# Kernel tuning notes

Measured on AMD Instinct MI355X. Metric: run time of the kernel, lower is better.

## Reference

```python
import jax, jax.numpy as jnp
import numpy as np

IN_F = 4096
OUT_F = 4096
BLOCK = 16      # weight values decoded per latent code
D_LAT = 16      # latent dim per code
HID = 64        # decoder hidden width
K = 65536       # codebook size
NB = IN_F * OUT_F // BLOCK  # 1,048,576 blocks


def setup_inputs() -> dict:
    key = jax.random.key(0)
    ks = jax.random.split(key, 10)
    return {
        "x": jax.random.normal(ks[0], (4, 2048, IN_F), jnp.float32),
        "y_in_idx": jax.random.randint(ks[1], (NB,), 0, K),
        "codebook": jax.random.normal(ks[2], (K, D_LAT), jnp.float32) * 0.1,
        "W1": jax.random.normal(ks[3], (D_LAT, HID), jnp.float32) * 0.1,
        "b1": jnp.zeros((HID,), jnp.float32),
        "W2": jax.random.normal(ks[4], (HID, BLOCK), jnp.float32) * 0.1,
        "b2": jnp.zeros((BLOCK,), jnp.float32),
        "scale": jax.random.uniform(ks[5], (OUT_F,), jnp.float32, 0.5, 1.5),
        "shift": jax.random.normal(ks[6], (OUT_F,), jnp.float32) * 0.01,
        "bias": jax.random.normal(ks[7], (OUT_F,), jnp.float32) * 0.02,
    }


def reference(x, y_in_idx, codebook, W1, b1, W2, b2, scale, shift, bias):
    # 1) gather latent codes for every weight block: [NB, D_LAT]
    codes = codebook[y_in_idx]
    # 2) decode latents -> weight blocks via small MLP (comp_W_from_y analogue)
    h = jax.nn.relu(codes @ W1 + b1)          # [NB, HID]
    blocks = h @ W2 + b2                      # [NB, BLOCK]
    # 3) assemble reconstructed (standardized) weight hatWr: [OUT_F, IN_F]
    Wr = blocks.reshape(OUT_F, IN_F)
    # 4) de-standardize with per-output-row metadata (de_standardize_Wr)
    W_hat = Wr * scale[:, None] + shift[:, None]
    # 5) F.linear(input, W_hat, bias): [B, S, OUT_F]
    return jnp.einsum('bsi,oi->bso', x, W_hat) + bias
```

## Files before the change

### kernel.cpp

```cpp
#include <hip/hip_runtime.h>
#include <hip/hip_bf16.h>

#define IN_F   4096
#define OUT_F  4096
#define HID    64
#define D_LAT  16
#define BLK    16
#define NB     (IN_F * OUT_F / BLK)
#define NCODES 65536
#define M_TOT  8192
#define K_TOT  IN_F
#define N_TOT  OUT_F

typedef __bf16 bf16x8 __attribute__((ext_vector_type(8)));
typedef float  f32x4  __attribute__((ext_vector_type(4)));

__global__ __launch_bounds__(256) void convert_x_kernel(
    const float* __restrict__ x, __hip_bfloat16* __restrict__ xb) {
  size_t i = ((size_t)blockIdx.x * 256 + threadIdx.x) * 8;
  const float4* p = (const float4*)(x + i);
  float4 a = p[0], b = p[1];
  union { __hip_bfloat16 h[8]; uint4 q; } u;
  u.h[0] = __float2bfloat16(a.x); u.h[1] = __float2bfloat16(a.y);
  u.h[2] = __float2bfloat16(a.z); u.h[3] = __float2bfloat16(a.w);
  u.h[4] = __float2bfloat16(b.x); u.h[5] = __float2bfloat16(b.y);
  u.h[6] = __float2bfloat16(b.z); u.h[7] = __float2bfloat16(b.w);
  *(uint4*)(xb + i) = u.q;
}

__global__ __launch_bounds__(256) void decode_table_kernel(
    const float* __restrict__ codebook,
    const float* __restrict__ W1, const float* __restrict__ b1,
    const float* __restrict__ W2, const float* __restrict__ b2,
    float* __restrict__ table) {
  __shared__ __align__(16) __hip_bfloat16 sH[4][16 * 72];
  const int lane = threadIdx.x & 63;
  const int wave = threadIdx.x >> 6;
  const int n = lane & 15;
  const int q = lane >> 4;
  const bool act = q < 2;

  union { __hip_bfloat16 h[8]; bf16x8 v; } uz;
#pragma unroll
  for (int j = 0; j < 8; j++) uz.h[j] = __float2bfloat16(0.f);
  const bf16x8 zf = uz.v;
  const f32x4 z4 = (f32x4){0.f, 0.f, 0.f, 0.f};

  bf16x8 frag1[4];
#pragma unroll
  for (int g = 0; g < 4; g++) {
    union { __hip_bfloat16 h[8]; bf16x8 v; } u;
#pragma unroll
    for (int j = 0; j < 8; j++) {
      int k = (q * 8 + j) & 15;
      float w = act ? W1[k * HID + g * 16 + n] : 0.f;
      u.h[j] = __float2bfloat16(w);
    }
    frag1[g] = u.v;
  }
  bf16x8 frag2[2];
#pragma unroll
  for (int kk = 0; kk < 2; kk++) {
    union { __hip_bfloat16 h[8]; bf16x8 v; } u;
#pragma unroll
    for (int j = 0; j < 8; j++)
      u.h[j] = __float2bfloat16(W2[(kk * 32 + q * 8 + j) * BLK + n]);
    frag2[kk] = u.v;
  }
  float b1v[4];
#pragma unroll
  for (int g = 0; g < 4; g++) b1v[g] = b1[g * 16 + n];
  const float b2v = b2[n];

  const int c0w = blockIdx.x * 256 + wave * 64;
#pragma unroll 1
  for (int i = 0; i < 4; i++) {
    const int cbase = c0w + i * 16;
    const int id = cbase + n;
    const float4* cp = (const float4*)(codebook + (size_t)id * D_LAT + (q & 1) * 8);
    float4 ca = cp[0], cb = cp[1];
    union { __hip_bfloat16 h[8]; bf16x8 v; } ua;
    ua.h[0] = __float2bfloat16(ca.x); ua.h[1] = __float2bfloat16(ca.y);
    ua.h[2] = __float2bfloat16(ca.z); ua.h[3] = __float2bfloat16(ca.w);
    ua.h[4] = __float2bfloat16(cb.x); ua.h[5] = __float2bfloat16(cb.y);
    ua.h[6] = __float2bfloat16(cb.z); ua.h[7] = __float2bfloat16(cb.w);
    bf16x8 afrag = act ? ua.v : zf;

    f32x4 hC[4];
#pragma unroll
    for (int g = 0; g < 4; g++)
      hC[g] = __builtin_amdgcn_mfma_f32_16x16x32_bf16(afrag, frag1[g], z4, 0, 0, 0);

    __syncthreads();
#pragma unroll
    for (int g = 0; g < 4; g++)
#pragma unroll
      for (int r = 0; r < 4; r++) {
        float hv = fmaxf(hC[g][r] + b1v[g], 0.f);
        sH[wave][(q * 4 + r) * 72 + g * 16 + n] = __float2bfloat16(hv);
      }
    __syncthreads();

    bf16x8 a2_0 = *(const bf16x8*)&sH[wave][n * 72 + q * 8];
    bf16x8 a2_1 = *(const bf16x8*)&sH[wave][n * 72 + 32 + q * 8];
    f32x4 o4 = __builtin_amdgcn_mfma_f32_16x16x32_bf16(a2_0, frag2[0], z4, 0, 0, 0);
    o4 = __builtin_amdgcn_mfma_f32_16x16x32_bf16(a2_1, frag2[1], o4, 0, 0, 0);

#pragma unroll
    for (int r = 0; r < 4; r++) {
      int code = cbase + q * 4 + r;
      table[(size_t)code * BLK + n] = o4[r] + b2v;
    }
  }
}

__global__ __launch_bounds__(256) void gather_scale_kernel(
    const int* __restrict__ yidx, const float* __restrict__ table,
    const float* __restrict__ scale, const float* __restrict__ shift,
    __hip_bfloat16* __restrict__ What) {
  const int b = blockIdx.x * 256 + threadIdx.x;
  const int o = blockIdx.x;
  const float sc = scale[o], sh = shift[o];
  const int id = yidx[b];
  const float4* t = (const float4*)(table + (size_t)id * BLK);
  float4 v0 = t[0], v1 = t[1], v2 = t[2], v3 = t[3];
  union { __hip_bfloat16 h[16]; uint4 q[2]; } u;
  u.h[0]  = __float2bfloat16(v0.x * sc + sh);
  u.h[1]  = __float2bfloat16(v0.y * sc + sh);
  u.h[2]  = __float2bfloat16(v0.z * sc + sh);
  u.h[3]  = __float2bfloat16(v0.w * sc + sh);
  u.h[4]  = __float2bfloat16(v1.x * sc + sh);
  u.h[5]  = __float2bfloat16(v1.y * sc + sh);
  u.h[6]  = __float2bfloat16(v1.z * sc + sh);
  u.h[7]  = __float2bfloat16(v1.w * sc + sh);
  u.h[8]  = __float2bfloat16(v2.x * sc + sh);
  u.h[9]  = __float2bfloat16(v2.y * sc + sh);
  u.h[10] = __float2bfloat16(v2.z * sc + sh);
  u.h[11] = __float2bfloat16(v2.w * sc + sh);
  u.h[12] = __float2bfloat16(v3.x * sc + sh);
  u.h[13] = __float2bfloat16(v3.y * sc + sh);
  u.h[14] = __float2bfloat16(v3.z * sc + sh);
  u.h[15] = __float2bfloat16(v3.w * sc + sh);
  uint4* dst = (uint4*)(What + (size_t)b * BLK);
  dst[0] = u.q[0];
  dst[1] = u.q[1];
}

__device__ inline void gload_lds16(const void* g, void* l) {
  __builtin_amdgcn_global_load_lds(
      (const __attribute__((address_space(1))) void*)g,
      (__attribute__((address_space(3))) void*)l, 16, 0, 0);
}

__global__ __launch_bounds__(256, 2) void gemm_bt_kernel(
    const __hip_bfloat16* __restrict__ A, const __hip_bfloat16* __restrict__ B,
    const float* __restrict__ bias, float* __restrict__ C) {
  __shared__ __align__(16) __hip_bfloat16 sA[256 * 32];
  __shared__ __align__(16) __hip_bfloat16 sB[128 * 32];
  const int lane = threadIdx.x & 63;
  const int wave = threadIdx.x >> 6;
  const int m0 = blockIdx.y * 256;
  const int n0 = blockIdx.x * 128;
  const int wr = wave >> 1;
  const int wc = wave & 1;

  const int srow = lane >> 2;
  const int schk = (lane & 3) ^ ((lane >> 3) & 3);
  const __hip_bfloat16* aSrc =
      A + (size_t)(m0 + wave * 64 + srow) * K_TOT + schk * 8;
  const __hip_bfloat16* bSrc =
      B + (size_t)(n0 + wave * 32 + srow) * K_TOT + schk * 8;

  const int fl = lane & 15;
  const int pos = (lane >> 4) ^ ((fl >> 1) & 3);
  const __hip_bfloat16* aRd = &sA[(wr * 128 + fl) * 32 + pos * 8];
  const __hip_bfloat16* bRd = &sB[(wc * 64 + fl) * 32 + pos * 8];

  f32x4 acc[8][4];
#pragma unroll
  for (int i = 0; i < 8; i++)
#pragma unroll
    for (int j = 0; j < 4; j++) acc[i][j] = (f32x4){0.f, 0.f, 0.f, 0.f};

  for (int k0 = 0; k0 < K_TOT; k0 += 32) {
#pragma unroll
    for (int i = 0; i < 4; i++)
      gload_lds16(aSrc + (size_t)i * 16 * K_TOT + k0,
                  (char*)sA + (wave * 4 + i) * 1024);
#pragma unroll
    for (int i = 0; i < 2; i++)
      gload_lds16(bSrc + (size_t)i * 16 * K_TOT + k0,
                  (char*)sB + (wave * 2 + i) * 1024);
    __syncthreads();

    bf16x8 bf[4];
#pragma unroll
    for (int nt = 0; nt < 4; nt++) bf[nt] = *(const bf16x8*)(bRd + nt * 16 * 32);
#pragma unroll
    for (int mt = 0; mt < 8; mt++) {
      bf16x8 af = *(const bf16x8*)(aRd + mt * 16 * 32);
#pragma unroll
      for (int nt = 0; nt < 4; nt++)
        acc[mt][nt] = __builtin_amdgcn_mfma_f32_16x16x32_bf16(
            af, bf[nt], acc[mt][nt], 0, 0, 0);
    }
    __syncthreads();
  }

  float bs[4];
#pragma unroll
  for (int nt = 0; nt < 4; nt++) bs[nt] = bias[n0 + wc * 64 + nt * 16 + fl];
#pragma unroll
  for (int mt = 0; mt < 8; mt++) {
    int r0 = m0 + wr * 128 + mt * 16 + (lane >> 4) * 4;
#pragma unroll
    for (int nt = 0; nt < 4; nt++) {
      int cn = n0 + wc * 64 + nt * 16 + fl;
#pragma unroll
      for (int r = 0; r < 4; r++)
        C[(size_t)(r0 + r) * N_TOT + cn] = acc[mt][nt][r] + bs[nt];
    }
  }
}

extern "C" void kernel_launch(void* const* d_in, const int* in_sizes, int n_in,
                              void* d_out, int out_size, void* d_ws, size_t ws_size,
                              hipStream_t stream) {
  const float* x        = (const float*)d_in[0];
  const int*   yidx     = (const int*)d_in[1];
  const float* codebook = (const float*)d_in[2];
  const float* W1       = (const float*)d_in[3];
  const float* b1       = (const float*)d_in[4];
  const float* W2       = (const float*)d_in[5];
  const float* b2       = (const float*)d_in[6];
  const float* scale    = (const float*)d_in[7];
  const float* shift    = (const float*)d_in[8];
  const float* bias     = (const float*)d_in[9];
  float* out = (float*)d_out;

  __hip_bfloat16* What = (__hip_bfloat16*)d_ws;
  float* table = (float*)((char*)d_ws + (size_t)32 * 1024 * 1024);
  __hip_bfloat16* xb   = (__hip_bfloat16*)((char*)d_ws + (size_t)32 * 1024 * 1024);

  decode_table_kernel<<<NCODES / 256, 256, 0, stream>>>(codebook, W1, b1, W2, b2,
                                                        table);
  gather_scale_kernel<<<NB / 256, 256, 0, stream>>>(yidx, table, scale, shift, What);
  convert_x_kernel<<<(M_TOT * (size_t)K_TOT) / (256 * 8), 256, 0, stream>>>(x, xb);
  gemm_bt_kernel<<<dim3(N_TOT / 128, M_TOT / 256), 256, 0, stream>>>(xb, What, bias, out);
}
```

Before: 530.1 us.

## Replace GEMM with 256x256-tile double-buffered 8-phase pipelined kernel

Rewrites the bf16 GEMM to use 512-thread workgroups, 256x256 output tiles and a 64-wide K step. The main loop is double-buffered in 128KB of LDS and split into eight phases that interleave global-to-LDS staging with LDS reads and MFMA blocks, using raw barriers, waitcnt and setprio. It also remaps block IDs for L2 locality and uses an XOR-swizzled LDS layout. The aim is to hide global load latency and raise MFMA utilisation compared with the single-buffered loop, which synchronised twice per 32-wide K step. The cost is much higher LDS use per workgroup and fragile hand-written wait counts.

```diff
diff --git a/kernel.cpp b/kernel.cpp
--- a/kernel.cpp
+++ b/kernel.cpp
@@ -11,9 +11,14 @@
 #define M_TOT  8192
 #define K_TOT  IN_F
 #define N_TOT  OUT_F
+#define NT     (K_TOT / 64)
 
 typedef __bf16 bf16x8 __attribute__((ext_vector_type(8)));
 typedef float  f32x4  __attribute__((ext_vector_type(4)));
+
+#define S_BARRIER()  asm volatile("s_barrier" ::: "memory")
+#define WAIT_LGKM0() asm volatile("s_waitcnt lgkmcnt(0)" ::: "memory")
+#define WAIT_VM(n)   asm volatile("s_waitcnt vmcnt(" #n ")" ::: "memory")
 
 __global__ __launch_bounds__(256) void convert_x_kernel(
     const float* __restrict__ x, __hip_bfloat16* __restrict__ xb) {
@@ -152,75 +157,153 @@
       (__attribute__((address_space(3))) void*)l, 16, 0, 0);
 }
 
-__global__ __launch_bounds__(256, 2) void gemm_bt_kernel(
+__global__ __launch_bounds__(512, 2) void gemm_8ph_kernel(
     const __hip_bfloat16* __restrict__ A, const __hip_bfloat16* __restrict__ B,
     const float* __restrict__ bias, float* __restrict__ C) {
-  __shared__ __align__(16) __hip_bfloat16 sA[256 * 32];
-  __shared__ __align__(16) __hip_bfloat16 sB[128 * 32];
-  const int lane = threadIdx.x & 63;
-  const int wave = threadIdx.x >> 6;
-  const int m0 = blockIdx.y * 256;
-  const int n0 = blockIdx.x * 128;
-  const int wr = wave >> 1;
-  const int wc = wave & 1;
-
-  const int srow = lane >> 2;
-  const int schk = (lane & 3) ^ ((lane >> 3) & 3);
-  const __hip_bfloat16* aSrc =
-      A + (size_t)(m0 + wave * 64 + srow) * K_TOT + schk * 8;
-  const __hip_bfloat16* bSrc =
-      B + (size_t)(n0 + wave * 32 + srow) * K_TOT + schk * 8;
-
+  __shared__ __align__(16) char ldsb[131072];
+  const int tid  = threadIdx.x;
+  const int lane = tid & 63;
+  const int wave = tid >> 6;
+  const int wm = wave >> 2;
+  const int wn = wave & 3;
   const int fl = lane & 15;
-  const int pos = (lane >> 4) ^ ((fl >> 1) & 3);
-  const __hip_bfloat16* aRd = &sA[(wr * 128 + fl) * 32 + pos * 8];
-  const __hip_bfloat16* bRd = &sB[(wc * 64 + fl) * 32 + pos * 8];
-
+  const int q  = lane >> 4;
+
+  const int bid = blockIdx.x;
+  const int wg  = (bid & 7) * 64 + (bid >> 3);
+  const int m0 = (wg >> 4) * 256;
+  const int n0 = (wg & 15) * 256;
+
+  const __hip_bfloat16* Ab = A + (size_t)m0 * K_TOT;
+  const __hip_bfloat16* Bb = B + (size_t)n0 * K_TOT;
+
+  const int r0s = tid >> 3;
+  const int r1s = r0s + 64;
+  const int cbs = ((tid & 7) << 4) ^ ((r0s & 7) << 4);
+  const size_t e0 = (size_t)r0s * K_TOT + (cbs >> 1);
+  const size_t e1 = (size_t)r1s * K_TOT + (cbs >> 1);
+
+  const int sw  = (fl & 7) << 4;
+  const int cA0 = (q * 16) ^ sw;
+  const int cA1 = (64 + q * 16) ^ sw;
+  const int aRow = (wm * 64 + fl) * 128;
+  const int bRow = 32768 + (wn * 32 + fl) * 128;
+
+#define STAGE_A(tt, hh, PP) do {                                               \
+    gload_lds16(Ab + (size_t)(hh) * 128 * K_TOT + (size_t)(tt) * 64 + e0,      \
+                ldsb + (PP) * 65536 + (hh) * 16384 + wave * 1024);             \
+    gload_lds16(Ab + (size_t)(hh) * 128 * K_TOT + (size_t)(tt) * 64 + e1,      \
+                ldsb + (PP) * 65536 + (hh) * 16384 + 8192 + wave * 1024);      \
+  } while (0)
+#define STAGE_B(tt, hh, PP) do {                                               \
+    gload_lds16(Bb + (size_t)(hh) * 128 * K_TOT + (size_t)(tt) * 64 + e0,      \
+                ldsb + (PP) * 65536 + 32768 + (hh) * 16384 + wave * 1024);     \
+    gload_lds16(Bb + (size_t)(hh) * 128 * K_TOT + (size_t)(tt) * 64 + e1,      \
+                ldsb + (PP) * 65536 + 32768 + (hh) * 16384 + 8192 + wave * 1024);\
+  } while (0)
+
+  bf16x8 aF[4][2], bF0[2][2], bF1[2][2];
   f32x4 acc[8][4];
 #pragma unroll
   for (int i = 0; i < 8; i++)
 #pragma unroll
     for (int j = 0; j < 4; j++) acc[i][j] = (f32x4){0.f, 0.f, 0.f, 0.f};
 
-  for (int k0 = 0; k0 < K_TOT; k0 += 32) {
-#pragma unroll
-    for (int i = 0; i < 4; i++)
-      gload_lds16(aSrc + (size_t)i * 16 * K_TOT + k0,
-                  (char*)sA + (wave * 4 + i) * 1024);
-#pragma unroll
-    for (int i = 0; i < 2; i++)
-      gload_lds16(bSrc + (size_t)i * 16 * K_TOT + k0,
-                  (char*)sB + (wave * 2 + i) * 1024);
-    __syncthreads();
-
-    bf16x8 bf[4];
-#pragma unroll
-    for (int nt = 0; nt < 4; nt++) bf[nt] = *(const bf16x8*)(bRd + nt * 16 * 32);
-#pragma unroll
-    for (int mt = 0; mt < 8; mt++) {
-      bf16x8 af = *(const bf16x8*)(aRd + mt * 16 * 32);
-#pragma unroll
-      for (int nt = 0; nt < 4; nt++)
-        acc[mt][nt] = __builtin_amdgcn_mfma_f32_16x16x32_bf16(
-            af, bf[nt], acc[mt][nt], 0, 0, 0);
-    }
-    __syncthreads();
+#define READ_A(PP, mh) do { _Pragma("unroll")                                  \
+    for (int mt = 0; mt < 4; ++mt) {                                           \
+      aF[mt][0] = *(const bf16x8*)(ldsb + (PP) * 65536 + (mh) * 16384 +        \
+                                   aRow + mt * 2048 + cA0);                    \
+      aF[mt][1] = *(const bf16x8*)(ldsb + (PP) * 65536 + (mh) * 16384 +        \
+                                   aRow + mt * 2048 + cA1);                    \
+    } } while (0)
+#define READ_B(PP, nh, DST) do { _Pragma("unroll")                             \
+    for (int nt = 0; nt < 2; ++nt) {                                           \
+      DST[nt][0] = *(const bf16x8*)(ldsb + (PP) * 65536 + (nh) * 16384 +       \
+                                    bRow + nt * 2048 + cA0);                   \
+      DST[nt][1] = *(const bf16x8*)(ldsb + (PP) * 65536 + (nh) * 16384 +       \
+                                    bRow + nt * 2048 + cA1);                   \
+    } } while (0)
+#define MFMA16(mh, nh, BF) do {                                                \
+    __builtin_amdgcn_s_setprio(1);                                             \
+    _Pragma("unroll") for (int mt = 0; mt < 4; ++mt)                           \
+    _Pragma("unroll") for (int nt = 0; nt < 2; ++nt) {                         \
+      f32x4 c = acc[(mh) * 4 + mt][(nh) * 2 + nt];                             \
+      c = __builtin_amdgcn_mfma_f32_16x16x32_bf16(aF[mt][0], BF[nt][0], c, 0, 0, 0); \
+      c = __builtin_amdgcn_mfma_f32_16x16x32_bf16(aF[mt][1], BF[nt][1], c, 0, 0, 0); \
+      acc[(mh) * 4 + mt][(nh) * 2 + nt] = c;                                   \
+    }                                                                          \
+    __builtin_amdgcn_s_setprio(0);                                             \
+  } while (0)
+
+  STAGE_A(0, 0, 0); STAGE_A(0, 1, 0); STAGE_B(0, 0, 0); STAGE_B(0, 1, 0);
+  STAGE_A(1, 0, 1); STAGE_A(1, 1, 1); STAGE_B(1, 0, 1);
+  WAIT_VM(6);
+  S_BARRIER();
+
+#pragma unroll 1
+  for (int t = 0; t < NT; t += 2) {
+    const bool s2 = (t + 2) < NT;
+    const bool s3 = (t + 3) < NT;
+    READ_A(0, 0); READ_B(0, 0, bF0);
+    STAGE_B(t + 1, 1, 1);
+    S_BARRIER(); WAIT_LGKM0();
+    MFMA16(0, 0, bF0);
+    S_BARRIER();
+    READ_B(0, 1, bF1);
+    if (s2) STAGE_A(t + 2, 0, 0);
+    S_BARRIER(); WAIT_LGKM0();
+    MFMA16(0, 1, bF1);
+    S_BARRIER();
+    READ_A(0, 1);
+    if (s2) STAGE_B(t + 2, 0, 0);
+    S_BARRIER(); WAIT_LGKM0();
+    MFMA16(1, 1, bF1);
+    S_BARRIER();
+    if (s2) { STAGE_A(t + 2, 1, 0); WAIT_VM(6); } else { WAIT_VM(0); }
+    S_BARRIER();
+    MFMA16(1, 0, bF0);
+    S_BARRIER();
+    READ_A(1, 0); READ_B(1, 0, bF0);
+    if (s2) STAGE_B(t + 2, 1, 0);
+    S_BARRIER(); WAIT_LGKM0();
+    MFMA16(0, 0, bF0);
+    S_BARRIER();
+    READ_B(1, 1, bF1);
+    if (s3) STAGE_A(t + 3, 0, 1);
+    S_BARRIER(); WAIT_LGKM0();
+    MFMA16(0, 1, bF1);
+    S_BARRIER();
+    READ_A(1, 1);
+    if (s3) STAGE_B(t + 3, 0, 1);
+    S_BARRIER(); WAIT_LGKM0();
+    MFMA16(1, 1, bF1);
+    S_BARRIER();
+    if (s3) { STAGE_A(t + 3, 1, 1); WAIT_VM(6); } else { WAIT_VM(0); }
+    S_BARRIER();
+    MFMA16(1, 0, bF0);
+    S_BARRIER();
   }
 
   float bs[4];
 #pragma unroll
-  for (int nt = 0; nt < 4; nt++) bs[nt] = bias[n0 + wc * 64 + nt * 16 + fl];
+  for (int nt = 0; nt < 4; nt++)
+    bs[nt] = bias[n0 + (nt >> 1) * 128 + wn * 32 + (nt & 1) * 16 + fl];
 #pragma unroll
   for (int mt = 0; mt < 8; mt++) {
-    int r0 = m0 + wr * 128 + mt * 16 + (lane >> 4) * 4;
+    int r0 = m0 + (mt >> 2) * 128 + wm * 64 + (mt & 3) * 16 + q * 4;
 #pragma unroll
     for (int nt = 0; nt < 4; nt++) {
-      int cn = n0 + wc * 64 + nt * 16 + fl;
+      int cn = n0 + (nt >> 1) * 128 + wn * 32 + (nt & 1) * 16 + fl;
 #pragma unroll
       for (int r = 0; r < 4; r++)
         C[(size_t)(r0 + r) * N_TOT + cn] = acc[mt][nt][r] + bs[nt];
     }
   }
+#undef STAGE_A
+#undef STAGE_B
+#undef READ_A
+#undef READ_B
+#undef MFMA16
 }
 
 extern "C" void kernel_launch(void* const* d_in, const int* in_sizes, int n_in,
@@ -246,5 +329,5 @@
                                                         table);
   gather_scale_kernel<<<NB / 256, 256, 0, stream>>>(yidx, table, scale, shift, What);
   convert_x_kernel<<<(M_TOT * (size_t)K_TOT) / (256 * 8), 256, 0, stream>>>(x, xb);
-  gemm_bt_kernel<<<dim3(N_TOT / 128, M_TOT / 256), 256, 0, stream>>>(xb, What, bias, out);
-}
+  gemm_8ph_kernel<<<512, 512, 0, stream>>>(xb, What, bias, out);
+}
```

New measurement: 484.3 us. -8.6%, faster.
